# Kernel optimization log

Hardware: AMD Instinct MI355X
Metric: run time of the kernel (lower is better)

The kernel has to match this reference:

```python
import jax, jax.numpy as jnp
import numpy as np

B, L, D, H, FF = 2, 4096, 512, 8, 2048
HD = D // H
EPS = 1e-5


def _layer_norm(x, g, b):
    mu = jnp.mean(x, axis=-1, keepdims=True)
    var = jnp.mean(jnp.square(x - mu), axis=-1, keepdims=True)
    return (x - mu) * jax.lax.rsqrt(var + EPS) * g + b


def setup_inputs() -> dict:
    key = jax.random.key(0)
    ks = jax.random.split(key, 16)
    s = 1.0 / np.sqrt(D)
    inp = {
        'x': jax.random.normal(ks[0], (B, L, D), dtype=jnp.float32),
        'Wq': jax.random.normal(ks[1], (D, D), dtype=jnp.float32) * s,
        'bq': jnp.zeros((D,), jnp.float32),
        'Wk': jax.random.normal(ks[2], (D, D), dtype=jnp.float32) * s,
        'bk': jnp.zeros((D,), jnp.float32),
        'Wv': jax.random.normal(ks[3], (D, D), dtype=jnp.float32) * s,
        'bv': jnp.zeros((D,), jnp.float32),
        'Wo': jax.random.normal(ks[4], (D, D), dtype=jnp.float32) * s,
        'bo': jnp.zeros((D,), jnp.float32),
        'ln1_g': jnp.ones((D,), jnp.float32),
        'ln1_b': jnp.zeros((D,), jnp.float32),
        'W1': jax.random.normal(ks[5], (D, FF), dtype=jnp.float32) * s,
        'b1': jnp.zeros((FF,), jnp.float32),
        'W2': jax.random.normal(ks[6], (FF, D), dtype=jnp.float32) * (1.0 / np.sqrt(FF)),
        'b2': jnp.zeros((D,), jnp.float32),
        'ln2_g': jnp.ones((D,), jnp.float32),
        'ln2_b': jnp.zeros((D,), jnp.float32),
        'window': 128,
    }
    return inp


def reference(x, Wq, bq, Wk, bk, Wv, bv, Wo, bo, ln1_g, ln1_b, W1, b1, W2, b2, ln2_g, ln2_b, window):
    # ---- local (banded) self-attention, matching nn.MultiheadAttention math ----
    q = (x @ Wq + bq).reshape(B, L, H, HD)
    k = (x @ Wk + bk).reshape(B, L, H, HD)
    v = (x @ Wv + bv).reshape(B, L, H, HD)
    scale = 1.0 / np.sqrt(HD)
    scores = jnp.einsum('bqhd,bkhd->bhqk', q, k) * scale  # [B,H,L,L]
    idx = jnp.arange(L)
    band = jnp.abs(idx[None, :] - idx[:, None]) > window   # True = masked
    scores = jnp.where(band[None, None], -jnp.inf, scores)
    probs = jax.nn.softmax(scores, axis=-1)
    attn = jnp.einsum('bhqk,bkhd->bqhd', probs, v).reshape(B, L, D)
    attn = attn @ Wo + bo
    # ---- residual + norm1 ----
    h = _layer_norm(x + attn, ln1_g, ln1_b)
    # ---- FFN + residual + norm2 (dropout=0 at eval) ----
    ff = jax.nn.relu(h @ W1 + b1) @ W2 + b2
    return _layer_norm(h + ff, ln2_g, ln2_b)
```

## Files before the change

### kernel.cpp

```cpp
#include <hip/hip_runtime.h>

namespace {

constexpr int B = 2, L = 4096, D = 512, H = 8, FF = 2048;
constexpr int M = B * L;
constexpr float LN_EPS = 1e-5f;

typedef __attribute__((ext_vector_type(8))) short short8;
typedef __attribute__((ext_vector_type(4))) float floatx4;

typedef __attribute__((address_space(3))) unsigned int lds_uint;
typedef const __attribute__((address_space(1))) unsigned int glob_uint;

__device__ __forceinline__ void gl_lds16(const unsigned short* g, unsigned short* l) {
  __builtin_amdgcn_global_load_lds((glob_uint*)g, (lds_uint*)l, 16, 0, 0);
}

__device__ __forceinline__ unsigned short f2bf(float f) {
  union { float f; unsigned u; } v; v.f = f;
  unsigned r = v.u + 0x7FFFu + ((v.u >> 16) & 1u);
  return (unsigned short)(r >> 16);
}

__global__ void k_prep(const float* __restrict__ x,
                       const float* __restrict__ Wq, const float* __restrict__ Wk,
                       const float* __restrict__ Wv, const float* __restrict__ Wo,
                       const float* __restrict__ W1, const float* __restrict__ W2,
                       const float* __restrict__ bq, const float* __restrict__ bk,
                       const float* __restrict__ bv,
                       unsigned short* __restrict__ Xb,
                       unsigned short* __restrict__ WqkvT,
                       unsigned short* __restrict__ WoT,
                       unsigned short* __restrict__ W1T,
                       unsigned short* __restrict__ W2T,
                       float* __restrict__ bqkv) {
  int tid = blockIdx.x * blockDim.x + threadIdx.x;
  if (tid < 1048576) {
    float4 v = ((const float4*)x)[tid];
    ushort4 o = make_ushort4(f2bf(v.x), f2bf(v.y), f2bf(v.z), f2bf(v.w));
    ((ushort4*)Xb)[tid] = o;
    return;
  }
  int u = tid - 1048576;
  if (u < 786432) {
    const float* src = (u < 262144) ? Wq : (u < 524288 ? Wk : Wv);
    int uu = u & 262143;
    int n = uu >> 9, k = uu & 511;
    WqkvT[u] = f2bf(src[k * 512 + n]);
    return;
  }
  u -= 786432;
  if (u < 262144) { int n = u >> 9, k = u & 511; WoT[u] = f2bf(Wo[k * 512 + n]); return; }
  u -= 262144;
  if (u < 1048576) { int n = u >> 9, k = u & 511; W1T[u] = f2bf(W1[k * 2048 + n]); return; }
  u -= 1048576;
  if (u < 1048576) { int n = u >> 11, k = u & 2047; W2T[u] = f2bf(W2[k * 512 + n]); return; }
  u -= 1048576;
  if (u < 1536) bqkv[u] = (u < 512) ? bq[u] : (u < 1024 ? bk[u - 512] : bv[u - 1024]);
}

template <int EPI>
__global__ __launch_bounds__(256, 3)
void k_gemm(const unsigned short* __restrict__ A, const unsigned short* __restrict__ BT,
            const float* __restrict__ bias, void* __restrict__ Cout,
            const int klen, const int N) {
  __shared__ unsigned short lA[128 * 32];
  __shared__ unsigned short lB[128 * 32];
  const int tid = threadIdx.x;
  const int wave = tid >> 6, lane = tid & 63;
  const int quad = lane >> 4, l16 = lane & 15;
  const int m0 = blockIdx.y * 128, n0 = blockIdx.x * 128;
  const int wm = (wave >> 1) * 64, wn = (wave & 1) * 64;
  const int kbeg = blockIdx.z * klen;
  const size_t Kdim = (size_t)klen * gridDim.z;

  const floatx4 fzero = {0.f, 0.f, 0.f, 0.f};
  floatx4 acc[4][4];
#pragma unroll
  for (int i = 0; i < 4; ++i)
#pragma unroll
    for (int j = 0; j < 4; ++j) acc[i][j] = fzero;

  const int r0 = tid >> 2, o0 = (tid & 3) * 8;
  const int r1 = (256 + tid) >> 2, o1 = (tid & 3) * 8;
  const unsigned short* Ag0 = A + (size_t)(m0 + r0) * Kdim + kbeg + o0;
  const unsigned short* Ag1 = A + (size_t)(m0 + r1) * Kdim + kbeg + o1;
  const unsigned short* Bg0 = BT + (size_t)(n0 + r0) * Kdim + kbeg + o0;
  const unsigned short* Bg1 = BT + (size_t)(n0 + r1) * Kdim + kbeg + o1;
  unsigned short* lA0 = &lA[wave * 512];
  unsigned short* lA1 = &lA[(4 + wave) * 512];
  unsigned short* lB0 = &lB[wave * 512];
  unsigned short* lB1 = &lB[(4 + wave) * 512];

  for (int kt = 0; kt < klen; kt += 32) {
    __syncthreads();
    gl_lds16(Ag0 + kt, lA0);
    gl_lds16(Ag1 + kt, lA1);
    gl_lds16(Bg0 + kt, lB0);
    gl_lds16(Bg1 + kt, lB1);
    __syncthreads();
    short8 af[4], bf[4];
#pragma unroll
    for (int i = 0; i < 4; ++i) af[i] = *(const short8*)&lA[(wm + i * 16 + l16) * 32 + quad * 8];
#pragma unroll
    for (int j = 0; j < 4; ++j) bf[j] = *(const short8*)&lB[(wn + j * 16 + l16) * 32 + quad * 8];
#pragma unroll
    for (int i = 0; i < 4; ++i)
#pragma unroll
      for (int j = 0; j < 4; ++j)
        acc[i][j] = __builtin_amdgcn_mfma_f32_16x16x32_bf16(af[i], bf[j], acc[i][j], 0, 0, 0);
  }

  float* outf = (float*)Cout + (size_t)blockIdx.z * M * N;
#pragma unroll
  for (int j = 0; j < 4; ++j) {
    const int col = n0 + wn + j * 16 + l16;
    const float bv = (blockIdx.z == 0) ? bias[col] : 0.f;
#pragma unroll
    for (int i = 0; i < 4; ++i) {
      const int row = m0 + wm + i * 16 + quad * 4;
#pragma unroll
      for (int r = 0; r < 4; ++r) {
        float v = acc[i][j][r] + bv;
        if (EPI == 1) v = fmaxf(v, 0.f);
        if (EPI == 2)
          outf[(size_t)(row + r) * N + col] = v;
        else
          ((unsigned short*)Cout)[(size_t)(row + r) * N + col] = f2bf(v);
      }
    }
  }
}

__global__ __launch_bounds__(256, 2)
void k_attn(const unsigned short* __restrict__ QKV, unsigned short* __restrict__ attnb,
            const int* __restrict__ wptr) {
  const int W = wptr[0];
  __shared__ unsigned short ldsP[4][16 * 40];
  const int tid = threadIdx.x;
  const int wave = tid >> 6, lane = tid & 63;
  const int quad = lane >> 4, l16 = lane & 15;
  const int blk = blockIdx.x;
  const int qt = blk & 63;
  const int h = (blk >> 6) & 7;
  const int b = blk >> 9;
  const int q0blk = qt * 64;
  const int q0 = q0blk + wave * 16;
  const float scale = 0.125f;

  const unsigned short* Qp = QKV + (size_t)(b * L + q0 + l16) * 1536 + h * 64;
  short8 qf0 = *(const short8*)(Qp + quad * 8);
  short8 qf1 = *(const short8*)(Qp + 32 + quad * 8);

  const floatx4 fzero = {0.f, 0.f, 0.f, 0.f};
  floatx4 o[4];
#pragma unroll
  for (int i = 0; i < 4; ++i) o[i] = fzero;
  float mrow[4] = {-1e30f, -1e30f, -1e30f, -1e30f};
  float lrow[4] = {0.f, 0.f, 0.f, 0.f};

  const unsigned short* Kbase = QKV + (size_t)(b * L) * 1536 + 512 + h * 64;
  const unsigned short* Vbase = QKV + (size_t)(b * L) * 1536 + 1024 + h * 64;
  unsigned short* lp = ldsP[wave];

  for (int it = 0; it < 10; ++it) {
    const int jb = q0blk - 128 + it * 32;
    __syncthreads();
    floatx4 s[2];
#pragma unroll
    for (int ct = 0; ct < 2; ++ct) {
      int key = jb + ct * 16 + l16;
      int keyc = key < 0 ? 0 : (key > L - 1 ? L - 1 : key);
      const unsigned short* Kr = Kbase + (size_t)keyc * 1536;
      floatx4 z = fzero;
      z = __builtin_amdgcn_mfma_f32_16x16x32_bf16(qf0, *(const short8*)(Kr + quad * 8), z, 0, 0, 0);
      z = __builtin_amdgcn_mfma_f32_16x16x32_bf16(qf1, *(const short8*)(Kr + 32 + quad * 8), z, 0, 0, 0);
      s[ct] = z;
    }
    const int key0 = jb + l16, key1 = jb + 16 + l16;
    const bool in0 = (key0 >= 0) && (key0 < L);
    const bool in1 = (key1 >= 0) && (key1 < L);
#pragma unroll
    for (int r = 0; r < 4; ++r) {
      int q = q0 + quad * 4 + r;
      int d0 = q - key0; d0 = d0 < 0 ? -d0 : d0;
      int d1 = q - key1; d1 = d1 < 0 ? -d1 : d1;
      bool ok0 = in0 && (d0 <= W);
      bool ok1 = in1 && (d1 <= W);
      float v0 = ok0 ? s[0][r] * scale : -1e30f;
      float v1 = ok1 ? s[1][r] * scale : -1e30f;
      float mx = fmaxf(v0, v1);
#pragma unroll
      for (int dd = 1; dd < 16; dd <<= 1) mx = fmaxf(mx, __shfl_xor(mx, dd, 64));
      float mnew = fmaxf(mrow[r], mx);
      float alpha = __expf(mrow[r] - mnew);
      float p0 = ok0 ? __expf(v0 - mnew) : 0.f;
      float p1 = ok1 ? __expf(v1 - mnew) : 0.f;
      float ps = p0 + p1;
#pragma unroll
      for (int dd = 1; dd < 16; dd <<= 1) ps += __shfl_xor(ps, dd, 64);
      lrow[r] = lrow[r] * alpha + ps;
      mrow[r] = mnew;
#pragma unroll
      for (int nt = 0; nt < 4; ++nt) o[nt][r] *= alpha;
      lp[(quad * 4 + r) * 40 + l16] = f2bf(p0);
      lp[(quad * 4 + r) * 40 + 16 + l16] = f2bf(p1);
    }
    __syncthreads();
    short8 af = *(const short8*)&lp[l16 * 40 + quad * 8];
    const unsigned short* vr[8];
#pragma unroll
    for (int j = 0; j < 8; ++j) {
      int key = jb + quad * 8 + j;
      int keyc = key < 0 ? 0 : (key > L - 1 ? L - 1 : key);
      vr[j] = Vbase + (size_t)keyc * 1536;
    }
#pragma unroll
    for (int nt = 0; nt < 4; ++nt) {
      short8 vf;
#pragma unroll
      for (int j = 0; j < 8; ++j) vf[j] = (short)vr[j][nt * 16 + l16];
      o[nt] = __builtin_amdgcn_mfma_f32_16x16x32_bf16(af, vf, o[nt], 0, 0, 0);
    }
  }
#pragma unroll
  for (int r = 0; r < 4; ++r) {
    float inv = 1.f / lrow[r];
    size_t base = (size_t)(b * L + q0 + quad * 4 + r) * 512 + h * 64;
#pragma unroll
    for (int nt = 0; nt < 4; ++nt)
      attnb[base + nt * 16 + l16] = f2bf(o[nt][r] * inv);
  }
}

template <int NP>
__global__ __launch_bounds__(256, 2)
void k_res_ln(const float* __restrict__ t0, const float* __restrict__ t1,
              const float* __restrict__ res,
              const float* __restrict__ gamma, const float* __restrict__ beta,
              float* __restrict__ outf, unsigned short* __restrict__ outb) {
  const int wave = threadIdx.x >> 6, lane = threadIdx.x & 63;
  const int row = blockIdx.x * 4 + wave;
  const float4* tv = (const float4*)(t0 + (size_t)row * D);
  const float4* rv = (const float4*)(res + (size_t)row * D);
  float4 a0 = tv[lane], a1 = tv[lane + 64];
  float4 b0 = rv[lane], b1 = rv[lane + 64];
  float4 y0 = make_float4(a0.x + b0.x, a0.y + b0.y, a0.z + b0.z, a0.w + b0.w);
  float4 y1 = make_float4(a1.x + b1.x, a1.y + b1.y, a1.z + b1.z, a1.w + b1.w);
  if (NP == 2) {
    const float4* uv = (const float4*)(t1 + (size_t)row * D);
    float4 c0 = uv[lane], c1 = uv[lane + 64];
    y0.x += c0.x; y0.y += c0.y; y0.z += c0.z; y0.w += c0.w;
    y1.x += c1.x; y1.y += c1.y; y1.z += c1.z; y1.w += c1.w;
  }
  float s = y0.x + y0.y + y0.z + y0.w + y1.x + y1.y + y1.z + y1.w;
  float q = y0.x * y0.x + y0.y * y0.y + y0.z * y0.z + y0.w * y0.w +
            y1.x * y1.x + y1.y * y1.y + y1.z * y1.z + y1.w * y1.w;
#pragma unroll
  for (int d = 1; d < 64; d <<= 1) {
    s += __shfl_xor(s, d, 64);
    q += __shfl_xor(q, d, 64);
  }
  const float mean = s * (1.f / D);
  const float var = q * (1.f / D) - mean * mean;
  const float rstd = rsqrtf(var + LN_EPS);
  float4 g0 = ((const float4*)gamma)[lane], g1 = ((const float4*)gamma)[lane + 64];
  float4 e0 = ((const float4*)beta)[lane], e1 = ((const float4*)beta)[lane + 64];
  float4 o0 = make_float4((y0.x - mean) * rstd * g0.x + e0.x, (y0.y - mean) * rstd * g0.y + e0.y,
                          (y0.z - mean) * rstd * g0.z + e0.z, (y0.w - mean) * rstd * g0.w + e0.w);
  float4 o1 = make_float4((y1.x - mean) * rstd * g1.x + e1.x, (y1.y - mean) * rstd * g1.y + e1.y,
                          (y1.z - mean) * rstd * g1.z + e1.z, (y1.w - mean) * rstd * g1.w + e1.w);
  ((float4*)(outf + (size_t)row * D))[lane] = o0;
  ((float4*)(outf + (size_t)row * D))[lane + 64] = o1;
  if (outb) {
    ((ushort4*)(outb + (size_t)row * D))[lane] =
        make_ushort4(f2bf(o0.x), f2bf(o0.y), f2bf(o0.z), f2bf(o0.w));
    ((ushort4*)(outb + (size_t)row * D))[lane + 64] =
        make_ushort4(f2bf(o1.x), f2bf(o1.y), f2bf(o1.z), f2bf(o1.w));
  }
}

}

extern "C" void kernel_launch(void* const* d_in, const int* in_sizes, int n_in,
                              void* d_out, int out_size, void* d_ws, size_t ws_size,
                              hipStream_t stream) {
  const float* x   = (const float*)d_in[0];
  const float* Wq  = (const float*)d_in[1];
  const float* bq  = (const float*)d_in[2];
  const float* Wk  = (const float*)d_in[3];
  const float* bk  = (const float*)d_in[4];
  const float* Wv  = (const float*)d_in[5];
  const float* bv  = (const float*)d_in[6];
  const float* Wo  = (const float*)d_in[7];
  const float* bo  = (const float*)d_in[8];
  const float* g1  = (const float*)d_in[9];
  const float* be1 = (const float*)d_in[10];
  const float* W1  = (const float*)d_in[11];
  const float* b1  = (const float*)d_in[12];
  const float* W2  = (const float*)d_in[13];
  const float* b2  = (const float*)d_in[14];
  const float* g2  = (const float*)d_in[15];
  const float* be2 = (const float*)d_in[16];
  const int* wptr  = (const int*)d_in[17];
  float* out = (float*)d_out;

  char* w = (char*)d_ws;
  size_t off = 0;
  auto take = [&](size_t bytes) -> void* {
    void* p = w + off;
    off += (bytes + 255) & ~(size_t)255;
    return p;
  };
  unsigned short* Xb    = (unsigned short*)take((size_t)M * D * 2);
  unsigned short* QKVb  = (unsigned short*)take((size_t)M * 1536 * 2);
  unsigned short* attnb = (unsigned short*)take((size_t)M * D * 2);
  unsigned short* WqkvT = (unsigned short*)take((size_t)1536 * 512 * 2);
  unsigned short* WoT   = (unsigned short*)take((size_t)512 * 512 * 2);
  unsigned short* W1T   = (unsigned short*)take((size_t)2048 * 512 * 2);
  unsigned short* W2T   = (unsigned short*)take((size_t)512 * 2048 * 2);
  float* bqkv           = (float*)take(1536 * 4);
  float* tbuf           = (float*)take((size_t)2 * M * D * 4);
  float* hbuf           = (float*)take((size_t)M * D * 4);
  unsigned short* hb    = (unsigned short*)take((size_t)M * D * 2);
  unsigned short* ffb   = (unsigned short*)take((size_t)M * FF * 2);

  k_prep<<<16390, 256, 0, stream>>>(x, Wq, Wk, Wv, Wo, W1, W2, bq, bk, bv,
                                    Xb, WqkvT, WoT, W1T, W2T, bqkv);
  k_gemm<0><<<dim3(12, 64, 1), 256, 0, stream>>>(Xb, WqkvT, bqkv, QKVb, 512, 1536);
  k_attn<<<B * H * (L / 64), 256, 0, stream>>>(QKVb, attnb, wptr);
  k_gemm<2><<<dim3(4, 64, 2), 256, 0, stream>>>(attnb, WoT, bo, tbuf, 256, 512);
  k_res_ln<2><<<M / 4, 256, 0, stream>>>(tbuf, tbuf + (size_t)M * D, x, g1, be1, hbuf, hb);
  k_gemm<1><<<dim3(16, 64, 1), 256, 0, stream>>>(hb, W1T, b1, ffb, 512, 2048);
  k_gemm<2><<<dim3(4, 64, 2), 256, 0, stream>>>(ffb, W2T, b2, tbuf, 1024, 512);
  k_res_ln<2><<<M / 4, 256, 0, stream>>>(tbuf, tbuf + (size_t)M * D, hbuf, g2, be2, out, nullptr);
}
```

Before: 282.0 us.

## Stage transposed V tile in LDS and widen attention key chunks to 64

```diff
diff --git a/kernel.cpp b/kernel.cpp
--- a/kernel.cpp
+++ b/kernel.cpp
@@ -132,22 +132,36 @@
   }
 }
 
-__global__ __launch_bounds__(256, 2)
+__global__ __launch_bounds__(256, 3)
 void k_attn(const unsigned short* __restrict__ QKV, unsigned short* __restrict__ attnb,
             const int* __restrict__ wptr) {
   const int W = wptr[0];
-  __shared__ unsigned short ldsP[4][16 * 40];
+  constexpr int VS = 324;
+  __shared__ unsigned short Vt[64 * VS];
+  __shared__ unsigned short Pb[4][16 * 72];
   const int tid = threadIdx.x;
   const int wave = tid >> 6, lane = tid & 63;
   const int quad = lane >> 4, l16 = lane & 15;
   const int blk = blockIdx.x;
-  const int qt = blk & 63;
-  const int h = (blk >> 6) & 7;
-  const int b = blk >> 9;
+  const int qt = blk & 63, h = (blk >> 6) & 7, b = blk >> 9;
   const int q0blk = qt * 64;
   const int q0 = q0blk + wave * 16;
   const float scale = 0.125f;
 
+  const unsigned short* Kbase = QKV + (size_t)(b * L) * 1536 + 512 + h * 64;
+  const unsigned short* Vbase = QKV + (size_t)(b * L) * 1536 + 1024 + h * 64;
+
+#pragma unroll
+  for (int i = 0; i < 10; ++i) {
+    int c = tid + i * 256;
+    int row = c >> 3, cd = (c & 7) * 8;
+    int key = q0blk - 128 + row;
+    int keyc = key < 0 ? 0 : (key > L - 1 ? L - 1 : key);
+    short8 v = *(const short8*)(Vbase + (size_t)keyc * 1536 + cd);
+#pragma unroll
+    for (int e = 0; e < 8; ++e) Vt[(cd + e) * VS + row] = (unsigned short)v[e];
+  }
+
   const unsigned short* Qp = QKV + (size_t)(b * L + q0 + l16) * 1536 + h * 64;
   short8 qf0 = *(const short8*)(Qp + quad * 8);
   short8 qf1 = *(const short8*)(Qp + 32 + quad * 8);
@@ -158,18 +172,16 @@
   for (int i = 0; i < 4; ++i) o[i] = fzero;
   float mrow[4] = {-1e30f, -1e30f, -1e30f, -1e30f};
   float lrow[4] = {0.f, 0.f, 0.f, 0.f};
-
-  const unsigned short* Kbase = QKV + (size_t)(b * L) * 1536 + 512 + h * 64;
-  const unsigned short* Vbase = QKV + (size_t)(b * L) * 1536 + 1024 + h * 64;
-  unsigned short* lp = ldsP[wave];
-
-  for (int it = 0; it < 10; ++it) {
-    const int jb = q0blk - 128 + it * 32;
-    __syncthreads();
-    floatx4 s[2];
-#pragma unroll
-    for (int ct = 0; ct < 2; ++ct) {
-      int key = jb + ct * 16 + l16;
+  unsigned short* lp = Pb[wave];
+
+  __syncthreads();
+
+  for (int it = 0; it < 5; ++it) {
+    const int jbg = q0blk - 128 + it * 64;
+    floatx4 s[4];
+#pragma unroll
+    for (int ct = 0; ct < 4; ++ct) {
+      int key = jbg + ct * 16 + l16;
       int keyc = key < 0 ? 0 : (key > L - 1 ? L - 1 : key);
       const unsigned short* Kr = Kbase + (size_t)keyc * 1536;
       floatx4 z = fzero;
@@ -177,50 +189,45 @@
       z = __builtin_amdgcn_mfma_f32_16x16x32_bf16(qf1, *(const short8*)(Kr + 32 + quad * 8), z, 0, 0, 0);
       s[ct] = z;
     }
-    const int key0 = jb + l16, key1 = jb + 16 + l16;
-    const bool in0 = (key0 >= 0) && (key0 < L);
-    const bool in1 = (key1 >= 0) && (key1 < L);
 #pragma unroll
     for (int r = 0; r < 4; ++r) {
       int q = q0 + quad * 4 + r;
-      int d0 = q - key0; d0 = d0 < 0 ? -d0 : d0;
-      int d1 = q - key1; d1 = d1 < 0 ? -d1 : d1;
-      bool ok0 = in0 && (d0 <= W);
-      bool ok1 = in1 && (d1 <= W);
-      float v0 = ok0 ? s[0][r] * scale : -1e30f;
-      float v1 = ok1 ? s[1][r] * scale : -1e30f;
-      float mx = fmaxf(v0, v1);
+      float v[4];
+      bool ok[4];
+      float mx = -1e30f;
+#pragma unroll
+      for (int ct = 0; ct < 4; ++ct) {
+        int key = jbg + ct * 16 + l16;
+        int d = q - key; d = d < 0 ? -d : d;
+        ok[ct] = (key >= 0) && (key < L) && (d <= W);
+        v[ct] = ok[ct] ? s[ct][r] * scale : -1e30f;
+        mx = fmaxf(mx, v[ct]);
+      }
 #pragma unroll
       for (int dd = 1; dd < 16; dd <<= 1) mx = fmaxf(mx, __shfl_xor(mx, dd, 64));
       float mnew = fmaxf(mrow[r], mx);
       float alpha = __expf(mrow[r] - mnew);
-      float p0 = ok0 ? __expf(v0 - mnew) : 0.f;
-      float p1 = ok1 ? __expf(v1 - mnew) : 0.f;
-      float ps = p0 + p1;
+      float ps = 0.f;
+#pragma unroll
+      for (int ct = 0; ct < 4; ++ct) {
+        float p = ok[ct] ? __expf(v[ct] - mnew) : 0.f;
+        ps += p;
+        lp[(quad * 4 + r) * 72 + ct * 16 + l16] = f2bf(p);
+      }
 #pragma unroll
       for (int dd = 1; dd < 16; dd <<= 1) ps += __shfl_xor(ps, dd, 64);
       lrow[r] = lrow[r] * alpha + ps;
       mrow[r] = mnew;
 #pragma unroll
       for (int nt = 0; nt < 4; ++nt) o[nt][r] *= alpha;
-      lp[(quad * 4 + r) * 40 + l16] = f2bf(p0);
-      lp[(quad * 4 + r) * 40 + 16 + l16] = f2bf(p1);
     }
-    __syncthreads();
-    short8 af = *(const short8*)&lp[l16 * 40 + quad * 8];
-    const unsigned short* vr[8];
-#pragma unroll
-    for (int j = 0; j < 8; ++j) {
-      int key = jb + quad * 8 + j;
-      int keyc = key < 0 ? 0 : (key > L - 1 ? L - 1 : key);
-      vr[j] = Vbase + (size_t)keyc * 1536;
-    }
+    short8 pf0 = *(const short8*)&lp[l16 * 72 + quad * 8];
+    short8 pf1 = *(const short8*)&lp[l16 * 72 + 32 + quad * 8];
 #pragma unroll
     for (int nt = 0; nt < 4; ++nt) {
-      short8 vf;
-#pragma unroll
-      for (int j = 0; j < 8; ++j) vf[j] = (short)vr[j][nt * 16 + l16];
-      o[nt] = __builtin_amdgcn_mfma_f32_16x16x32_bf16(af, vf, o[nt], 0, 0, 0);
+      const unsigned short* vp = &Vt[(nt * 16 + l16) * VS + it * 64 + quad * 8];
+      o[nt] = __builtin_amdgcn_mfma_f32_16x16x32_bf16(pf0, *(const short8*)vp, o[nt], 0, 0, 0);
+      o[nt] = __builtin_amdgcn_mfma_f32_16x16x32_bf16(pf1, *(const short8*)(vp + 32), o[nt], 0, 0, 0);
     }
   }
 #pragma unroll
```

Result: faster. 274.6 us (-2.6%).
